# Performance work log

Measured on AMD Instinct MI355X. Metric: run time of the kernel, lower is better.

## Reference

```python
import jax, jax.numpy as jnp
import numpy as np

B, T, E, H = 8, 2048, 1024, 64

def setup_inputs() -> dict:
    key = jax.random.key(0)
    ks = jax.random.split(key, 7)
    s = 1.0 / np.sqrt(E)
    return {
        "x": jax.random.normal(ks[0], (B, T, E), dtype=jnp.float32),
        "Wk": jax.random.normal(ks[1], (E, H), dtype=jnp.float32) * s,
        "bk": jax.random.normal(ks[2], (H,), dtype=jnp.float32) * 0.01,
        "Wq": jax.random.normal(ks[3], (E, H), dtype=jnp.float32) * s,
        "bq": jax.random.normal(ks[4], (H,), dtype=jnp.float32) * 0.01,
        "Wv": jax.random.normal(ks[5], (E, H), dtype=jnp.float32) * s,
        "bv": jax.random.normal(ks[6], (H,), dtype=jnp.float32) * 0.01,
    }

def reference(x, Wk, bk, Wq, bq, Wv, bv):
    # q,k,v: [B, T, H]
    k = x @ Wk + bk
    q = x @ Wq + bq
    v = x @ Wv + bv
    scale = jnp.asarray(H, x.dtype) ** -0.5
    scores = jnp.einsum('bth,bsh->bts', q, k) * scale  # [B, T, T]
    T_ = x.shape[1]
    causal = jnp.tril(jnp.ones((T_, T_), dtype=bool))
    scores = jnp.where(causal, scores, jnp.asarray(-jnp.inf, x.dtype))
    attn = jax.nn.softmax(scores, axis=-1)  # dropout p=0.0 -> identity
    return jnp.einsum('bts,bsh->bth', attn, v)
```

## Files before the change

### kernel.cpp

```cpp
#include <hip/hip_runtime.h>
#include <hip/hip_bf16.h>
#include <math.h>

#define BB 8
#define TT 2048
#define EE 1024
#define HH 64
#define QSCALE 0.18033688011112042f

typedef __attribute__((ext_vector_type(8))) short short8;
typedef __attribute__((ext_vector_type(4))) float f32x4;
typedef __attribute__((ext_vector_type(4))) unsigned short us4;

__device__ inline unsigned short f2bf(float f) {
  union { __hip_bfloat16 h; unsigned short u; } cv;
  cv.h = __float2bfloat16(f);
  return cv.u;
}

__global__ __launch_bounds__(256) void prep_w(
    const float* __restrict__ Wk, const float* __restrict__ Wq,
    const float* __restrict__ Wv, unsigned short* __restrict__ Wf) {
  const int idx = blockIdx.x * 256 + threadIdx.x;
  const int lane = idx & 63, ks = (idx >> 6) & 31, t = idx >> 11;
  const int q = lane & 15, g = lane >> 4;
  const int m = t >> 2, h = (t & 3) * 16 + q;
  const float* W = (m == 0) ? Wk : (m == 1) ? Wq : Wv;
  const float sc = (m == 1) ? QSCALE : 1.f;
  const int e0 = ks * 32 + g * 8;
  unsigned short v[8];
  #pragma unroll
  for (int j = 0; j < 8; ++j) v[j] = f2bf(W[(e0 + j) * 64 + h] * sc);
  *(short8*)&Wf[(size_t)idx * 8] = *(short8*)v;
}

__global__ __launch_bounds__(256) void qkv_proj(
    const float* __restrict__ x,
    const float* __restrict__ bk, const float* __restrict__ bq,
    const float* __restrict__ bv, const unsigned short* __restrict__ Wf,
    unsigned short* __restrict__ kf, unsigned short* __restrict__ qf,
    unsigned short* __restrict__ vf) {
  __shared__ alignas(16) unsigned short xs[2][16][264];

  const int tid = threadIdx.x;
  const long row0 = (long)blockIdx.x * 16;
  const int w = tid >> 6, lane = tid & 63;
  const int q = lane & 15, g = lane >> 4;

  const float4* xg = (const float4*)&x[row0 * EE];

  #pragma unroll
  for (int i = 0; i < 4; ++i) {
    const int flat = i * 256 + tid;
    const int rr = flat >> 6, c4 = flat & 63;
    const float4 xv = xg[rr * 256 + c4];
    us4 pk = {f2bf(xv.x), f2bf(xv.y), f2bf(xv.z), f2bf(xv.w)};
    *(us4*)&xs[0][rr][c4 * 4] = pk;
  }
  __syncthreads();

  const f32x4 z = {0.f, 0.f, 0.f, 0.f};
  f32x4 acc0 = z, acc1 = z, acc2 = z;
  const unsigned short* wf0 = &Wf[(size_t)w * 16384 + (size_t)lane * 8];

  float4 st[4];
  #pragma unroll
  for (int cc = 0; cc < 4; ++cc) {
    if (cc < 3) {
      #pragma unroll
      for (int i = 0; i < 4; ++i) {
        const int flat = i * 256 + tid;
        const int rr = flat >> 6, c4 = flat & 63;
        st[i] = xg[rr * 256 + (cc + 1) * 64 + c4];
      }
    }
    #pragma unroll
    for (int ksl = 0; ksl < 8; ++ksl) {
      const short8 af = *(const short8*)&xs[cc & 1][q][ksl * 32 + g * 8];
      const int ks = cc * 8 + ksl;
      const short8 b0 = *(const short8*)&wf0[ks * 512];
      const short8 b1 = *(const short8*)&wf0[65536 + ks * 512];
      const short8 b2 = *(const short8*)&wf0[131072 + ks * 512];
      acc0 = __builtin_amdgcn_mfma_f32_16x16x32_bf16(af, b0, acc0, 0, 0, 0);
      acc1 = __builtin_amdgcn_mfma_f32_16x16x32_bf16(af, b1, acc1, 0, 0, 0);
      acc2 = __builtin_amdgcn_mfma_f32_16x16x32_bf16(af, b2, acc2, 0, 0, 0);
    }
    if (cc < 3) {
      #pragma unroll
      for (int i = 0; i < 4; ++i) {
        const int flat = i * 256 + tid;
        const int rr = flat >> 6, c4 = flat & 63;
        us4 pk = {f2bf(st[i].x), f2bf(st[i].y), f2bf(st[i].z), f2bf(st[i].w)};
        *(us4*)&xs[(cc + 1) & 1][rr][c4 * 4] = pk;
      }
    }
    __syncthreads();
  }

  const int h = w * 16 + q;
  const float biask = bk[h], biasq = bq[h] * QSCALE, biasv = bv[h];
  const long bidx = row0 >> 11;
  const int tl0 = (int)(row0 & 2047);
  const int halfh = h >> 5, g2 = (h & 31) >> 3, jj = h & 7;
  const size_t kqbase = (size_t)bidx * 131072 + (size_t)(tl0 >> 4) * 1024 +
                        (size_t)halfh * 512 + (size_t)g2 * 128 + jj;
  #pragma unroll
  for (int r = 0; r < 4; ++r) {
    const int kq = 4 * g + r;
    kf[kqbase + kq * 8] = f2bf(acc0[r] + biask);
    qf[kqbase + kq * 8] = f2bf(acc1[r] + biasq);
    const int tl = tl0 + 4 * g + r;
    const size_t vidx = (size_t)bidx * 131072 + (size_t)(tl >> 5) * 2048 +
                        (size_t)(h >> 4) * 512 + (size_t)((tl & 31) >> 3) * 128 +
                        (size_t)(h & 15) * 8 + (tl & 7);
    vf[vidx] = f2bf(acc2[r] + biasv);
  }
}

#define BODY(KC0, KC1, KC2, KC3, KN0, KN1, KN2, KN3, tt, PREF) do {          \
    const unsigned short* vp_ = vfb + (size_t)(tt) * 2048;                   \
    const short8 V0 = *(const short8*)&vp_[0];                               \
    const short8 V1 = *(const short8*)&vp_[512];                             \
    const short8 V2 = *(const short8*)&vp_[1024];                            \
    const short8 V3 = *(const short8*)&vp_[1536];                            \
    if (PREF) {                                                              \
      const unsigned short* kp_ = kfb + (size_t)((tt) + stride) * 2048;      \
      KN0 = *(const short8*)&kp_[0];                                         \
      KN1 = *(const short8*)&kp_[512];                                       \
      KN2 = *(const short8*)&kp_[1024];                                      \
      KN3 = *(const short8*)&kp_[1536];                                      \
    }                                                                        \
    f32x4 sa = __builtin_amdgcn_mfma_f32_16x16x32_bf16(KC0, Qf0, z, 0,0,0);  \
    sa = __builtin_amdgcn_mfma_f32_16x16x32_bf16(KC1, Qf1, sa, 0,0,0);       \
    f32x4 sb = __builtin_amdgcn_mfma_f32_16x16x32_bf16(KC2, Qf0, z, 0,0,0);  \
    sb = __builtin_amdgcn_mfma_f32_16x16x32_bf16(KC3, Qf1, sb, 0,0,0);       \
    const int k0_ = (tt) * 32;                                               \
    if (k0_ + 31 > q0) {                                                     \
      _Pragma("unroll")                                                      \
      for (int r = 0; r < 4; ++r) {                                          \
        if (k0_ + 4 * g + r > qg) sa[r] = -INFINITY;                         \
        if (k0_ + 16 + 4 * g + r > qg) sb[r] = -INFINITY;                    \
      }                                                                      \
    }                                                                        \
    float pmax = fmaxf(fmaxf(fmaxf(sa[0], sa[1]), fmaxf(sa[2], sa[3])),      \
                       fmaxf(fmaxf(sb[0], sb[1]), fmaxf(sb[2], sb[3])));     \
    if (!__all(pmax <= m + 8.0f)) {                                          \
      float tmax = pmax;                                                     \
      tmax = fmaxf(tmax, __shfl_xor(tmax, 16));                              \
      tmax = fmaxf(tmax, __shfl_xor(tmax, 32));                              \
      const float nm = fmaxf(m, tmax);                                       \
      const float rs = __builtin_amdgcn_exp2f(m - nm);                       \
      l *= rs; o0 *= rs; o1 *= rs; o2 *= rs; o3 *= rs;                       \
      m = nm;                                                                \
    }                                                                        \
    float ps = 0.f;                                                          \
    _Pragma("unroll")                                                        \
    for (int r = 0; r < 4; ++r) {                                            \
      sa[r] = __builtin_amdgcn_exp2f(sa[r] - m); ps += sa[r];                \
      sb[r] = __builtin_amdgcn_exp2f(sb[r] - m); ps += sb[r];                \
    }                                                                        \
    l += ps;                                                                 \
    unsigned pw0, pw1, pw2, pw3;                                             \
    asm("v_cvt_pk_bf16_f32 %0, %1, %2" : "=v"(pw0) : "v"(sa[0]), "v"(sa[1]));\
    asm("v_cvt_pk_bf16_f32 %0, %1, %2" : "=v"(pw1) : "v"(sa[2]), "v"(sa[3]));\
    asm("v_cvt_pk_bf16_f32 %0, %1, %2" : "=v"(pw2) : "v"(sb[0]), "v"(sb[1]));\
    asm("v_cvt_pk_bf16_f32 %0, %1, %2" : "=v"(pw3) : "v"(sb[2]), "v"(sb[3]));\
    const int srcA = q + ((g & 1) << 5);                                     \
    const int srcB = srcA + 16;                                              \
    const unsigned r0a = __shfl((int)pw0, srcA);                             \
    const unsigned r1a = __shfl((int)pw1, srcA);                             \
    const unsigned r2a = __shfl((int)pw2, srcA);                             \
    const unsigned r3a = __shfl((int)pw3, srcA);                             \
    const unsigned r0b = __shfl((int)pw0, srcB);                             \
    const unsigned r1b = __shfl((int)pw1, srcB);                             \
    const unsigned r2b = __shfl((int)pw2, srcB);                             \
    const unsigned r3b = __shfl((int)pw3, srcB);                             \
    union { unsigned u[4]; short8 s; } pf_;                                  \
    const bool hi_ = (g >= 2);                                               \
    pf_.u[0] = hi_ ? r2a : r0a;                                              \
    pf_.u[1] = hi_ ? r3a : r1a;                                              \
    pf_.u[2] = hi_ ? r2b : r0b;                                              \
    pf_.u[3] = hi_ ? r3b : r1b;                                              \
    const short8 Pf = pf_.s;                                                 \
    o0 = __builtin_amdgcn_mfma_f32_16x16x32_bf16(V0, Pf, o0, 0,0,0);         \
    o1 = __builtin_amdgcn_mfma_f32_16x16x32_bf16(V1, Pf, o1, 0,0,0);         \
    o2 = __builtin_amdgcn_mfma_f32_16x16x32_bf16(V2, Pf, o2, 0,0,0);         \
    o3 = __builtin_amdgcn_mfma_f32_16x16x32_bf16(V3, Pf, o3, 0,0,0);         \
  } while (0)

__global__ __launch_bounds__(512) void attn_fwd(
    const unsigned short* __restrict__ qf, const unsigned short* __restrict__ kf,
    const unsigned short* __restrict__ vf, float* __restrict__ out) {
  __shared__ float accS[8][64][17];
  __shared__ float mlS[8][2][16];

  const int tid = threadIdx.x;
  const int w = tid >> 6, lane = tid & 63;
  const int q = lane & 15, g = lane >> 4;

  const int b = blockIdx.x & 7;
  const int p = blockIdx.x >> 3;
  const int s1 = 127 - p;
  const int nt0 = (p + 2) >> 1, nt1 = (129 - p) >> 1;
  int k = (8 * nt0 + 32) / 65;
  if (k < 1) k = 1;
  if (k > 7) k = 7;

  const bool onS0 = (w < k);
  const int s = onS0 ? p : s1;
  const int nt = onS0 ? nt0 : nt1;
  const int stride = onS0 ? k : (8 - k);
  int t = onS0 ? w : (w - k);

  const int q0 = s * 16;
  const int qg = q0 + q;

  const unsigned short* kfb = kf + (size_t)b * 131072 + (size_t)lane * 8;
  const unsigned short* vfb = vf + (size_t)b * 131072 + (size_t)lane * 8;
  const unsigned short* qfb = qf + (size_t)b * 131072 + (size_t)s * 1024 +
                              (size_t)lane * 8;
  const short8 Qf0 = *(const short8*)&qfb[0];
  const short8 Qf1 = *(const short8*)&qfb[512];

  const f32x4 z = {0.f, 0.f, 0.f, 0.f};
  float m = -3.0e38f, l = 0.f;
  f32x4 o0 = z, o1 = z, o2 = z, o3 = z;

  {
    short8 A0, A1, A2, A3, B0, B1, B2, B3;
    const unsigned short* kp0 = kfb + (size_t)t * 2048;
    A0 = *(const short8*)&kp0[0];
    A1 = *(const short8*)&kp0[512];
    A2 = *(const short8*)&kp0[1024];
    A3 = *(const short8*)&kp0[1536];
    for (;;) {
      bool pf = (t + stride) < nt;
      BODY(A0, A1, A2, A3, B0, B1, B2, B3, t, pf);
      if (!pf) break;
      t += stride;
      pf = (t + stride) < nt;
      BODY(B0, B1, B2, B3, A0, A1, A2, A3, t, pf);
      if (!pf) break;
      t += stride;
    }
  }

  float lq = l;
  lq += __shfl_xor(lq, 16);
  lq += __shfl_xor(lq, 32);
  #pragma unroll
  for (int hb = 0; hb < 4; ++hb) {
    const f32x4 a = (hb == 0) ? o0 : (hb == 1) ? o1 : (hb == 2) ? o2 : o3;
    #pragma unroll
    for (int r = 0; r < 4; ++r) accS[w][16 * hb + 4 * g + r][q] = a[r];
  }
  if (g == 0) { mlS[w][0][q] = m; mlS[w][1][q] = lq; }
  __syncthreads();

  const int half = tid >> 8;
  const int sm = half ? s1 : p;
  const int lo = half ? k : 0, hi = half ? 8 : k;
  const int row = tid & 63, qq = (tid >> 6) & 3;
  const long obase = ((long)b * TT + sm * 16) * 64;
  #pragma unroll
  for (int kk = 0; kk < 4; ++kk) {
    const int qv = qq + 4 * kk;
    float M = -INFINITY;
    for (int i = lo; i < hi; ++i) M = fmaxf(M, mlS[i][0][qv]);
    float L = 0.f, acc = 0.f;
    for (int i = lo; i < hi; ++i) {
      const float fi = __builtin_amdgcn_exp2f(mlS[i][0][qv] - M);
      L += fi * mlS[i][1][qv];
      acc += fi * accS[i][row][qv];
    }
    out[obase + (long)qv * 64 + row] = acc / L;
  }
}

extern "C" void kernel_launch(void* const* d_in, const int* in_sizes, int n_in,
                              void* d_out, int out_size, void* d_ws, size_t ws_size,
                              hipStream_t stream) {
  const float* x  = (const float*)d_in[0];
  const float* Wk = (const float*)d_in[1];
  const float* bk = (const float*)d_in[2];
  const float* Wq = (const float*)d_in[3];
  const float* bq = (const float*)d_in[4];
  const float* Wv = (const float*)d_in[5];
  const float* bv = (const float*)d_in[6];
  float* out = (float*)d_out;

  unsigned short* qfb = (unsigned short*)d_ws;
  unsigned short* kfb = qfb + (size_t)1048576;
  unsigned short* vfb = kfb + (size_t)1048576;
  unsigned short* Wf  = vfb + (size_t)1048576;

  prep_w<<<dim3(96), 256, 0, stream>>>(Wk, Wq, Wv, Wf);
  qkv_proj<<<dim3(1024), 256, 0, stream>>>(x, bk, bq, bv, Wf, kfb, qfb, vfb);
  attn_fwd<<<dim3(512), 512, 0, stream>>>(qfb, kfb, vfb, out);
}
```

Baseline: 50.82 us.

## Double row tile in QKV projection so each wave reuses weight fragments across two row blocks

Each QKV projection block now handles 32 rows instead of 16, and the grid drops from 1024 to 512 blocks. Each wave now owns three of the twelve 16-column output tiles and applies every loaded weight fragment to two 16-row A fragments. This halves global weight traffic per row and doubles MFMA work per weight load. The cost is more registers and LDS per block and fewer blocks to spread across the GPU.

```diff
diff --git a/kernel.cpp b/kernel.cpp
--- a/kernel.cpp
+++ b/kernel.cpp
@@ -40,17 +40,17 @@
     const float* __restrict__ bv, const unsigned short* __restrict__ Wf,
     unsigned short* __restrict__ kf, unsigned short* __restrict__ qf,
     unsigned short* __restrict__ vf) {
-  __shared__ alignas(16) unsigned short xs[2][16][264];
+  __shared__ alignas(16) unsigned short xs[2][32][264];
 
   const int tid = threadIdx.x;
-  const long row0 = (long)blockIdx.x * 16;
+  const long row0 = (long)blockIdx.x * 32;
   const int w = tid >> 6, lane = tid & 63;
   const int q = lane & 15, g = lane >> 4;
 
   const float4* xg = (const float4*)&x[row0 * EE];
 
   #pragma unroll
-  for (int i = 0; i < 4; ++i) {
+  for (int i = 0; i < 8; ++i) {
     const int flat = i * 256 + tid;
     const int rr = flat >> 6, c4 = flat & 63;
     const float4 xv = xg[rr * 256 + c4];
@@ -60,15 +60,16 @@
   __syncthreads();
 
   const f32x4 z = {0.f, 0.f, 0.f, 0.f};
-  f32x4 acc0 = z, acc1 = z, acc2 = z;
-  const unsigned short* wf0 = &Wf[(size_t)w * 16384 + (size_t)lane * 8];
-
-  float4 st[4];
+  f32x4 acc00 = z, acc01 = z, acc02 = z;
+  f32x4 acc10 = z, acc11 = z, acc12 = z;
+  const unsigned short* wf0 = &Wf[(size_t)(3 * w) * 16384 + (size_t)lane * 8];
+
+  float4 st[8];
   #pragma unroll
   for (int cc = 0; cc < 4; ++cc) {
     if (cc < 3) {
       #pragma unroll
-      for (int i = 0; i < 4; ++i) {
+      for (int i = 0; i < 8; ++i) {
         const int flat = i * 256 + tid;
         const int rr = flat >> 6, c4 = flat & 63;
         st[i] = xg[rr * 256 + (cc + 1) * 64 + c4];
@@ -76,18 +77,22 @@
     }
     #pragma unroll
     for (int ksl = 0; ksl < 8; ++ksl) {
-      const short8 af = *(const short8*)&xs[cc & 1][q][ksl * 32 + g * 8];
+      const short8 a0 = *(const short8*)&xs[cc & 1][q][ksl * 32 + g * 8];
+      const short8 a1 = *(const short8*)&xs[cc & 1][16 + q][ksl * 32 + g * 8];
       const int ks = cc * 8 + ksl;
       const short8 b0 = *(const short8*)&wf0[ks * 512];
-      const short8 b1 = *(const short8*)&wf0[65536 + ks * 512];
-      const short8 b2 = *(const short8*)&wf0[131072 + ks * 512];
-      acc0 = __builtin_amdgcn_mfma_f32_16x16x32_bf16(af, b0, acc0, 0, 0, 0);
-      acc1 = __builtin_amdgcn_mfma_f32_16x16x32_bf16(af, b1, acc1, 0, 0, 0);
-      acc2 = __builtin_amdgcn_mfma_f32_16x16x32_bf16(af, b2, acc2, 0, 0, 0);
+      const short8 b1 = *(const short8*)&wf0[16384 + ks * 512];
+      const short8 b2 = *(const short8*)&wf0[32768 + ks * 512];
+      acc00 = __builtin_amdgcn_mfma_f32_16x16x32_bf16(a0, b0, acc00, 0, 0, 0);
+      acc10 = __builtin_amdgcn_mfma_f32_16x16x32_bf16(a1, b0, acc10, 0, 0, 0);
+      acc01 = __builtin_amdgcn_mfma_f32_16x16x32_bf16(a0, b1, acc01, 0, 0, 0);
+      acc11 = __builtin_amdgcn_mfma_f32_16x16x32_bf16(a1, b1, acc11, 0, 0, 0);
+      acc02 = __builtin_amdgcn_mfma_f32_16x16x32_bf16(a0, b2, acc02, 0, 0, 0);
+      acc12 = __builtin_amdgcn_mfma_f32_16x16x32_bf16(a1, b2, acc12, 0, 0, 0);
     }
     if (cc < 3) {
       #pragma unroll
-      for (int i = 0; i < 4; ++i) {
+      for (int i = 0; i < 8; ++i) {
         const int flat = i * 256 + tid;
         const int rr = flat >> 6, c4 = flat & 63;
         us4 pk = {f2bf(st[i].x), f2bf(st[i].y), f2bf(st[i].z), f2bf(st[i].w)};
@@ -97,23 +102,37 @@
     __syncthreads();
   }
 
-  const int h = w * 16 + q;
-  const float biask = bk[h], biasq = bq[h] * QSCALE, biasv = bv[h];
   const long bidx = row0 >> 11;
   const int tl0 = (int)(row0 & 2047);
-  const int halfh = h >> 5, g2 = (h & 31) >> 3, jj = h & 7;
-  const size_t kqbase = (size_t)bidx * 131072 + (size_t)(tl0 >> 4) * 1024 +
-                        (size_t)halfh * 512 + (size_t)g2 * 128 + jj;
-  #pragma unroll
-  for (int r = 0; r < 4; ++r) {
-    const int kq = 4 * g + r;
-    kf[kqbase + kq * 8] = f2bf(acc0[r] + biask);
-    qf[kqbase + kq * 8] = f2bf(acc1[r] + biasq);
-    const int tl = tl0 + 4 * g + r;
-    const size_t vidx = (size_t)bidx * 131072 + (size_t)(tl >> 5) * 2048 +
-                        (size_t)(h >> 4) * 512 + (size_t)((tl & 31) >> 3) * 128 +
-                        (size_t)(h & 15) * 8 + (tl & 7);
-    vf[vidx] = f2bf(acc2[r] + biasv);
+  #pragma unroll
+  for (int i = 0; i < 3; ++i) {
+    const int tgl = 3 * w + i;
+    const int mm = tgl >> 2, hb = tgl & 3;
+    const int h = hb * 16 + q;
+    const float bias = (mm == 0) ? bk[h] : (mm == 1) ? bq[h] * QSCALE : bv[h];
+    #pragma unroll
+    for (int stp = 0; stp < 2; ++stp) {
+      const f32x4 a = (stp == 0) ? ((i == 0) ? acc00 : (i == 1) ? acc01 : acc02)
+                                 : ((i == 0) ? acc10 : (i == 1) ? acc11 : acc12);
+      #pragma unroll
+      for (int r = 0; r < 4; ++r) {
+        const int tl = tl0 + stp * 16 + 4 * g + r;
+        const unsigned short ov = f2bf(a[r] + bias);
+        if (mm == 2) {
+          const size_t vidx = (size_t)bidx * 131072 + (size_t)(tl >> 5) * 2048 +
+                              (size_t)(h >> 4) * 512 +
+                              (size_t)((tl & 31) >> 3) * 128 +
+                              (size_t)(h & 15) * 8 + (tl & 7);
+          vf[vidx] = ov;
+        } else {
+          const size_t kqidx = (size_t)bidx * 131072 + (size_t)(tl >> 4) * 1024 +
+                               (size_t)(h >> 5) * 512 +
+                               (size_t)((h & 31) >> 3) * 128 +
+                               (size_t)(tl & 15) * 8 + (h & 7);
+          if (mm == 0) kf[kqidx] = ov; else qf[kqidx] = ov;
+        }
+      }
+    }
   }
 }
 
@@ -295,6 +314,6 @@
   unsigned short* Wf  = vfb + (size_t)1048576;
 
   prep_w<<<dim3(96), 256, 0, stream>>>(Wk, Wq, Wv, Wf);
-  qkv_proj<<<dim3(1024), 256, 0, stream>>>(x, bk, bq, bv, Wf, kfb, qfb, vfb);
+  qkv_proj<<<dim3(512), 256, 0, stream>>>(x, bk, bq, bv, Wf, kfb, qfb, vfb);
   attn_fwd<<<dim3(512), 512, 0, stream>>>(qfb, kfb, vfb, out);
 }
```

After: 50.36 us. Within noise of the previous version (-0.9%).
